# Performance work log

Measured on AMD Instinct MI355X. Metric: run time of the kernel, lower is better.

Reference implementation:

```python
import jax, jax.numpy as jnp
import numpy as np

DIM = 256
NUM_RFS = 256
OUT_DIM = 1024
N = 65536
M = 0.001


def setup_inputs() -> dict:
    key = jax.random.key(0)
    k1, k2, k3, k4, k5, k6 = jax.random.split(key, 6)
    x = jax.random.normal(k1, (N, DIM), dtype=jnp.float32)
    input_weights = jax.random.normal(k2, (OUT_DIM, DIM), dtype=jnp.float32)
    b = jax.random.normal(k3, (OUT_DIM,), dtype=jnp.float32)
    # projection matrix: normal(mean=0, std=0.02, size=(num_rfs, dim))
    proj = 0.02 * jax.random.normal(k4, (NUM_RFS, DIM), dtype=jnp.float32)
    # xis are complex points of the random-feature construction; keep small for exp stability
    xis_real = 0.1 * jax.random.normal(k5, (NUM_RFS,), dtype=jnp.float32)
    xis_imag = 0.1 * jax.random.normal(k6, (NUM_RFS,), dtype=jnp.float32)
    return {"x": x, "input_weights": input_weights, "b": b, "proj": proj,
            "xis_real": xis_real, "xis_imag": xis_imag}


def _asym_feats(xw, xis, proj, bias, is_weight):
    """create_asym_feats with a_fun/b_fun = identity, A_fun/B_fun = exp(xi*b).
    xw: (rows, DIM) float; xis: (NUM_RFS,) complex64; proj: (NUM_RFS, DIM) float.
    Returns (rows, NUM_RFS) complex64."""
    ab = xis  # ab_fun is identity -> ab_coeffs = xis
    scale = np.sqrt(1.0 + 4.0 * M).astype(np.float32)
    # renorm_gs[i] = sqrt(1+4M) * ab[i] * gs[i]  -> (NUM_RFS, DIM) complex
    renorm_gs = scale * ab[:, None] * proj.astype(jnp.complex64)
    # dot_products = xw_c @ renorm_gs.T  -> (rows, NUM_RFS) complex
    dot = jnp.einsum('nd,rd->nr', xw.astype(jnp.complex64), renorm_gs)
    sq = jnp.sum(xw * xw, axis=-1)  # (rows,)
    # correction: outer(sq/2, ab*ab) + M*||g_i||^2 (broadcast over rows)
    corr = (sq[:, None] * 0.5) * (ab * ab)[None, :]
    corr = corr + M * jnp.sum(proj * proj, axis=-1)[None, :]
    feats = jnp.exp(dot - corr) * np.float32(1.0 / np.sqrt(NUM_RFS))
    if is_weight:
        # AB_coeffs[j, i] = exp(xis[i] * bias[j])
        AB = jnp.exp(xis[None, :] * bias[:, None].astype(jnp.complex64))
        feats = AB * feats
    return feats


def reference(x, input_weights, b, proj, xis_real, xis_imag):
    xis = (xis_real + 1j * xis_imag).astype(jnp.complex64)
    # normalize=False path: scale weights and bias by dim**-0.25 at init time
    inv4 = np.float32(1.0 / DIM ** 0.25)
    w = input_weights * inv4
    bb = b * inv4
    c = np.float32((1.0 / np.sqrt(2.0)) * (1.0 + 4.0 * M) ** (DIM / 4.0))
    # precomputed weight features (parameter of the module)
    w_plus = _asym_feats(w, xis, proj, bb, is_weight=True)
    w_minus = _asym_feats(w, -xis, proj, bb, is_weight=True)
    weights = c * jnp.concatenate([w_plus, w_minus], axis=-1)  # (OUT_DIM, 2R) complex
    # forward: x scaled by 1/dim (normalize=False)
    xs = x * np.float32(1.0 / DIM)
    f_plus = _asym_feats(xs, xis, proj, bb, is_weight=False)
    f_minus = _asym_feats(xs, -xis, proj, bb, is_weight=False)
    feat = c * jnp.concatenate([f_plus, f_minus], axis=-1)  # (N, 2R) complex
    # (feat @ weights.T).real
    out = jnp.einsum('nr,or->no', feat, weights).real
    return out
```

## Files before the change

kernel.cpp:

```cpp
#include <hip/hip_runtime.h>
#include <cmath>
#include <cstdint>

#define NROWS 65536
#define DIMN  256
#define NRF   256
#define OUTD  1024
#define KDIM  1024
#define MCOEF 0.001f

typedef __bf16 v8bf __attribute__((ext_vector_type(8)));
typedef float  v4f  __attribute__((ext_vector_type(4)));
typedef unsigned short us8 __attribute__((ext_vector_type(8)));

__device__ __forceinline__ unsigned short f2bf(float f) {
  unsigned int u = __float_as_uint(f);
  u += 0x7fffu + ((u >> 16) & 1u);
  return (unsigned short)(u >> 16);
}

__device__ __forceinline__ void async_copy16(const void* g, void* l) {
  __builtin_amdgcn_global_load_lds(
      (const __attribute__((address_space(1))) void*)g,
      (__attribute__((address_space(3))) void*)l, 16, 0, 0);
}

__device__ __forceinline__ int sw_slot(int r, int c) {
  return r * 4 + ((c ^ (r >> 1)) & 3);
}

__global__ __launch_bounds__(64) void prep_rf(
    const float* __restrict__ proj, unsigned short* __restrict__ projbf,
    float* __restrict__ mg2) {
  int i = blockIdx.x;
  int lane = threadIdx.x;
  float4 v = ((const float4*)(proj + (size_t)i * DIMN))[lane];
  ushort4 o;
  o.x = f2bf(v.x); o.y = f2bf(v.y); o.z = f2bf(v.z); o.w = f2bf(v.w);
  ((ushort4*)(projbf + (size_t)i * DIMN))[lane] = o;
  float ss = v.x * v.x + v.y * v.y + v.z * v.z + v.w * v.w;
#pragma unroll
  for (int off = 32; off > 0; off >>= 1) ss += __shfl_down(ss, off, 64);
  if (lane == 0) mg2[i] = MCOEF * ss;
}

__global__ __launch_bounds__(256) void fused_features(
    const float* __restrict__ srcX,
    const float* __restrict__ srcW,
    const float* __restrict__ biasW,
    const float* __restrict__ xr_g, const float* __restrict__ xi_g,
    const float* __restrict__ mg2_g,
    const unsigned short* __restrict__ projbf,
    unsigned short* __restrict__ FX,
    unsigned short* __restrict__ FW,
    float sRx, float sRw, float scaleC) {
  __shared__ __align__(16) unsigned short big[16 * 1024];
  unsigned short* As = big;
  unsigned short* Bs = big + 2048;
  unsigned short* Os = big;
  __shared__ float xr_s[256], xi_s[256], c1_s[256], c2_s[256], mg2_s[256];
  __shared__ float sq_s[64], bias_s[64];

  int t = threadIdx.x;
  int lane = t & 63;
  int w = t >> 6;

  bool isW = blockIdx.x < (OUTD / 64);
  int blockRow = isW ? blockIdx.x * 64 : (blockIdx.x - OUTD / 64) * 64;
  const float* src = isW ? srcW : srcX;
  float scl = isW ? 0.25f : (1.f / DIMN);
  unsigned short* Fout = isW ? FW : FX;
  float sR = isW ? sRw : sRx;
  float sI = isW ? -sRw : sRx;

  {
    float a = xr_g[t], b = xi_g[t];
    xr_s[t] = a; xi_s[t] = b;
    c1_s[t] = a * a - b * b;
    c2_s[t] = 2.f * a * b;
    mg2_s[t] = mg2_g[t];
  }
  if (t < 64) bias_s[t] = isW ? biasW[blockRow + t] * 0.25f : 0.f;

  v4f acc[4][4];
#pragma unroll
  for (int a = 0; a < 4; a++)
#pragma unroll
    for (int b = 0; b < 4; b++)
#pragma unroll
      for (int q = 0; q < 4; q++) acc[a][b][q] = 0.f;

  int arow = t >> 2, sub = t & 3;
  const float* srow = src + (size_t)(blockRow + arow) * DIMN + sub * 8;
  float ss = 0.f;

  for (int kb = 0; kb < DIMN; kb += 32) {
    float4 v0 = *(const float4*)(srow + kb);
    float4 v1 = *(const float4*)(srow + kb + 4);
    v0.x *= scl; v0.y *= scl; v0.z *= scl; v0.w *= scl;
    v1.x *= scl; v1.y *= scl; v1.z *= scl; v1.w *= scl;
    ss += v0.x * v0.x + v0.y * v0.y + v0.z * v0.z + v0.w * v0.w +
          v1.x * v1.x + v1.y * v1.y + v1.z * v1.z + v1.w * v1.w;
    us8 o;
    o[0] = f2bf(v0.x); o[1] = f2bf(v0.y); o[2] = f2bf(v0.z); o[3] = f2bf(v0.w);
    o[4] = f2bf(v1.x); o[5] = f2bf(v1.y); o[6] = f2bf(v1.z); o[7] = f2bf(v1.w);
    *(us8*)&As[sw_slot(arow, sub) * 8] = o;
#pragma unroll
    for (int r = 0; r < 4; r++) {
      int idx = r * 256 + t;
      int row = idx >> 2, kc = ((idx & 3) ^ ((idx >> 3) & 3)) * 8;
      async_copy16(projbf + (size_t)row * DIMN + kb + kc,
                   Bs + (idx & ~63) * 8);
    }
    __syncthreads();
    v8bf af[4], bfv[4];
    int c = lane >> 4;
#pragma unroll
    for (int mi = 0; mi < 4; mi++)
      af[mi] = *(const v8bf*)&As[sw_slot(mi * 16 + (lane & 15), c) * 8];
#pragma unroll
    for (int ni = 0; ni < 4; ni++)
      bfv[ni] = *(const v8bf*)&Bs[sw_slot(w * 64 + ni * 16 + (lane & 15), c) * 8];
#pragma unroll
    for (int mi = 0; mi < 4; mi++)
#pragma unroll
      for (int ni = 0; ni < 4; ni++)
        acc[mi][ni] = __builtin_amdgcn_mfma_f32_16x16x32_bf16(
            af[mi], bfv[ni], acc[mi][ni], 0, 0, 0);
    __syncthreads();
  }

  ss += __shfl_xor(ss, 1, 64);
  ss += __shfl_xor(ss, 2, 64);
  if (sub == 0) sq_s[arow] = ss;

#pragma unroll
  for (int mi = 0; mi < 4; mi++) {
    __syncthreads();
#pragma unroll
    for (int ni = 0; ni < 4; ni++) {
      int i = w * 64 + ni * 16 + (lane & 15);
      float xrv = xr_s[i], xiv = xi_s[i];
      float c1v = c1_s[i], c2v = c2_s[i], mgv = mg2_s[i];
#pragma unroll
      for (int reg = 0; reg < 4; reg++) {
        int rl    = (lane >> 4) * 4 + reg;
        int rglob = mi * 16 + rl;
        float px = acc[mi][ni][reg];
        float tt = scaleC * px + bias_s[rglob];
        float u  = 0.5f * sq_s[rglob];
        float aa = u * c1v + mgv;
        float bb = u * c2v;
        float txr = tt * xrv;
        float txi = tt * xiv;
        float erp = __expf(txr - aa);
        float erm = __expf(-txr - aa);
        float s1, cc1, s2, cc2;
        __sincosf(txi - bb, &s1, &cc1);
        __sincosf(txi + bb, &s2, &cc2);
        ushort4 ov;
        ov.x = f2bf(sR * erp * cc1);
        ov.y = f2bf(sR * erm * cc2);
        ov.z = f2bf(sI * erp * s1);
        ov.w = f2bf(-sI * erm * s2);
        *(ushort4*)&Os[rl * KDIM + 4 * i] = ov;
      }
    }
    __syncthreads();
#pragma unroll
    for (int j = 0; j < 8; j++) {
      int chunk = j * 256 + t;
      int rowo  = chunk >> 7;
      int off   = (chunk & 127) * 8;
      *(us8*)(Fout + (size_t)(blockRow + mi * 16 + rowo) * KDIM + off) =
          *(const us8*)&Os[rowo * KDIM + off];
    }
  }
}

#define WAITV(N) asm volatile("s_waitcnt vmcnt(" #N ")" ::: "memory")

__global__ __launch_bounds__(512) void gemm_bt(
    const unsigned short* __restrict__ A,
    const unsigned short* __restrict__ B,
    float* __restrict__ C) {
  __shared__ __align__(16) unsigned short As[2][256 * 64];
  __shared__ __align__(16) unsigned short Bs[2][256 * 64];
  int tt = threadIdx.x;
  int lane = tt & 63;
  int wv = tt >> 6;
  int wm = wv >> 2, wn = wv & 3;

  int lid = blockIdx.x;
  int wg = (lid & 7) * 128 + (lid >> 3);
  size_t bm = (size_t)(wg >> 2) * 256;
  size_t bn = (size_t)(wg & 3) * 256;

  unsigned int offA[2][2], offB[2][2];
#pragma unroll
  for (int h = 0; h < 2; h++)
#pragma unroll
    for (int i = 0; i < 2; i++) {
      int L = i * 512 + tt;
      int rho = h * 128 + (L >> 3);
      int c = (L & 7) ^ (rho & 7);
      int gA = ((rho >> 6) & 1) * 128 + (rho >> 7) * 64 + (rho & 63);
      int gB = ((rho >> 5) & 3) * 64 + (rho >> 7) * 32 + (rho & 31);
      offA[h][i] = (unsigned int)((bm + gA) * KDIM + c * 8);
      offB[h][i] = (unsigned int)((bn + gB) * KDIM + c * 8);
    }

#define STAGE_A(H, KB) do { \
  _Pragma("unroll") for (int i_ = 0; i_ < 2; i_++) \
    async_copy16(A + offA[H][i_] + (KB), \
                 &As[nbuf][((H) * 1024 + i_ * 512 + (tt & ~63)) * 8]); \
} while (0)
#define STAGE_B(H, KB) do { \
  _Pragma("unroll") for (int i_ = 0; i_ < 2; i_++) \
    async_copy16(B + offB[H][i_] + (KB), \
                 &Bs[nbuf][((H) * 1024 + i_ * 512 + (tt & ~63)) * 8]); \
} while (0)

  v8bf af[4][2], b0[2][2], b1[2][2];
  v4f acc[8][4];
#pragma unroll
  for (int a = 0; a < 8; a++)
#pragma unroll
    for (int b = 0; b < 4; b++)
#pragma unroll
      for (int q = 0; q < 4; q++) acc[a][b][q] = 0.f;

#define READ_A(MH) do { \
  _Pragma("unroll") for (int mf_ = 0; mf_ < 4; mf_++) { \
    int rho_ = (MH) * 128 + wm * 64 + mf_ * 16 + (lane & 15); \
    int sw_ = rho_ & 7; \
    const unsigned short* rp_ = &As[buf][rho_ * 64]; \
    af[mf_][0] = *(const v8bf*)&rp_[(((lane >> 4)) ^ sw_) * 8]; \
    af[mf_][1] = *(const v8bf*)&rp_[((4 + (lane >> 4)) ^ sw_) * 8]; \
  } \
} while (0)
#define READ_B(NH, DST) do { \
  _Pragma("unroll") for (int nf_ = 0; nf_ < 2; nf_++) { \
    int rho_ = (NH) * 128 + wn * 32 + nf_ * 16 + (lane & 15); \
    int sw_ = rho_ & 7; \
    const unsigned short* rp_ = &Bs[buf][rho_ * 64]; \
    DST[nf_][0] = *(const v8bf*)&rp_[(((lane >> 4)) ^ sw_) * 8]; \
    DST[nf_][1] = *(const v8bf*)&rp_[((4 + (lane >> 4)) ^ sw_) * 8]; \
  } \
} while (0)
#define MMA_Q(MH, NH, BSRC) do { \
  __builtin_amdgcn_s_setprio(1); \
  _Pragma("unroll") for (int mf_ = 0; mf_ < 4; mf_++) \
  _Pragma("unroll") for (int nf_ = 0; nf_ < 2; nf_++) \
  _Pragma("unroll") for (int ks_ = 0; ks_ < 2; ks_++) \
    acc[(MH) * 4 + mf_][(NH) * 2 + nf_] = \
        __builtin_amdgcn_mfma_f32_16x16x32_bf16( \
            af[mf_][ks_], BSRC[nf_][ks_], \
            acc[(MH) * 4 + mf_][(NH) * 2 + nf_], 0, 0, 0); \
  __builtin_amdgcn_s_setprio(0); \
} while (0)

  {
    const int nbuf = 0;
    STAGE_A(0, 0); STAGE_B(0, 0); STAGE_B(1, 0); STAGE_A(1, 0);
  }
  WAITV(4);
  __builtin_amdgcn_s_barrier();

  for (int t = 0; t < 16; ++t) {
    const int buf = t & 1, nbuf = buf ^ 1;
    const bool pf = (t < 15);
    const int kb = (t + 1) * 64;

    READ_A(0); READ_B(0, b0);
    if (pf) STAGE_A(0, kb);
    __builtin_amdgcn_s_barrier();
    MMA_Q(0, 0, b0);
    if (pf) { WAITV(4); } else { WAITV(2); }
    __builtin_amdgcn_s_barrier();

    READ_B(1, b1);
    if (pf) STAGE_B(0, kb);
    __builtin_amdgcn_s_barrier();
    MMA_Q(0, 1, b1);
    if (pf) { WAITV(4); } else { WAITV(0); }
    __builtin_amdgcn_s_barrier();

    READ_A(1);
    if (pf) STAGE_B(1, kb);
    __builtin_amdgcn_s_barrier();
    MMA_Q(1, 1, b1);
    __builtin_amdgcn_s_barrier();

    if (pf) STAGE_A(1, kb);
    __builtin_amdgcn_s_barrier();
    MMA_Q(1, 0, b0);
    if (pf) { WAITV(4); }
    __builtin_amdgcn_s_barrier();
  }

#pragma unroll
  for (int mf = 0; mf < 8; mf++)
#pragma unroll
    for (int nf = 0; nf < 4; nf++)
#pragma unroll
      for (int reg = 0; reg < 4; reg++) {
        size_t row = bm + wm * 128 + mf * 16 + (lane >> 4) * 4 + reg;
        size_t col = bn + wn * 64 + nf * 16 + (lane & 15);
        C[row * OUTD + col] = acc[mf][nf][reg];
      }
#undef STAGE_A
#undef STAGE_B
#undef READ_A
#undef READ_B
#undef MMA_Q
}

extern "C" void kernel_launch(void* const* d_in, const int* in_sizes, int n_in,
                              void* d_out, int out_size, void* d_ws, size_t ws_size,
                              hipStream_t stream) {
  (void)in_sizes; (void)n_in; (void)out_size;
  const float* x    = (const float*)d_in[0];
  const float* iw   = (const float*)d_in[1];
  const float* bvec = (const float*)d_in[2];
  const float* proj = (const float*)d_in[3];
  const float* xr   = (const float*)d_in[4];
  const float* xi   = (const float*)d_in[5];
  float* out = (float*)d_out;

  char* ws = (char*)d_ws;
  size_t off = 0;
  auto take = [&](size_t bytes) {
    char* p = ws + off;
    off = (off + bytes + 255) & ~(size_t)255;
    return p;
  };
  unsigned short* F      = (unsigned short*)take((size_t)NROWS * KDIM * 2);
  unsigned short* Wp     = (unsigned short*)take((size_t)OUTD * KDIM * 2);
  unsigned short* projbf = (unsigned short*)take((size_t)NRF * DIMN * 2);
  float* mg2 = (float*)take((size_t)NRF * 4);
  if (ws_size < off) return;

  const float  scaleC = sqrtf(1.f + 4.f * MCOEF);
  const double c2d    = 0.5 * exp(128.0 * log(1.0 + 4.0 * 0.001));
  const float  invSR  = 0.0625f;
  const float  sRw    = (float)(c2d * 0.0625);

  prep_rf<<<NRF, 64, 0, stream>>>(proj, projbf, mg2);
  fused_features<<<NROWS / 64 + OUTD / 64, 256, 0, stream>>>(
      x, iw, bvec, xr, xi, mg2, projbf, F, Wp, invSR, sRw, scaleC);
  gemm_bt<<<1024, 512, 0, stream>>>(F, Wp, out);
}
```

Before: 506.8 us.

## Double-buffer feature-kernel K loop and store features directly to global

Splits the A and B LDS tiles of the fused feature kernel into two buffers. The next K slice can then be staged while MFMAs run on the current one, removing one barrier per iteration. It also drops the LDS staging of the bf16 output tile and writes each 8-byte feature group straight to global memory, removing the per-row-block barriers and LDS round trip. The trade-offs are more LDS per block, which may lower occupancy, and narrower, less coalesced global stores.

```diff
diff --git a/kernel.cpp b/kernel.cpp
--- a/kernel.cpp
+++ b/kernel.cpp
@@ -54,10 +54,8 @@
     unsigned short* __restrict__ FX,
     unsigned short* __restrict__ FW,
     float sRx, float sRw, float scaleC) {
-  __shared__ __align__(16) unsigned short big[16 * 1024];
-  unsigned short* As = big;
-  unsigned short* Bs = big + 2048;
-  unsigned short* Os = big;
+  __shared__ __align__(16) unsigned short As[2][64 * 32];
+  __shared__ __align__(16) unsigned short Bs[2][256 * 32];
   __shared__ float xr_s[256], xi_s[256], c1_s[256], c2_s[256], mg2_s[256];
   __shared__ float sq_s[64], bias_s[64];
 
@@ -94,7 +92,16 @@
   const float* srow = src + (size_t)(blockRow + arow) * DIMN + sub * 8;
   float ss = 0.f;
 
-  for (int kb = 0; kb < DIMN; kb += 32) {
+  auto stageB = [&](int nb, int kb) {
+#pragma unroll
+    for (int r = 0; r < 4; r++) {
+      int idx = r * 256 + t;
+      int row = idx >> 2, kc = ((idx & 3) ^ ((idx >> 3) & 3)) * 8;
+      async_copy16(projbf + (size_t)row * DIMN + kb + kc,
+                   &Bs[nb][(idx & ~63) * 8]);
+    }
+  };
+  auto stageA = [&](int nb, int kb) {
     float4 v0 = *(const float4*)(srow + kb);
     float4 v1 = *(const float4*)(srow + kb + 4);
     v0.x *= scl; v0.y *= scl; v0.z *= scl; v0.w *= scl;
@@ -104,23 +111,27 @@
     us8 o;
     o[0] = f2bf(v0.x); o[1] = f2bf(v0.y); o[2] = f2bf(v0.z); o[3] = f2bf(v0.w);
     o[4] = f2bf(v1.x); o[5] = f2bf(v1.y); o[6] = f2bf(v1.z); o[7] = f2bf(v1.w);
-    *(us8*)&As[sw_slot(arow, sub) * 8] = o;
-#pragma unroll
-    for (int r = 0; r < 4; r++) {
-      int idx = r * 256 + t;
-      int row = idx >> 2, kc = ((idx & 3) ^ ((idx >> 3) & 3)) * 8;
-      async_copy16(projbf + (size_t)row * DIMN + kb + kc,
-                   Bs + (idx & ~63) * 8);
+    *(us8*)&As[nb][sw_slot(arow, sub) * 8] = o;
+  };
+
+  stageB(0, 0);
+  stageA(0, 0);
+  __syncthreads();
+
+  for (int kb = 0; kb < 8; kb++) {
+    int cur = kb & 1, nb = cur ^ 1;
+    if (kb < 7) {
+      stageB(nb, (kb + 1) * 32);
+      stageA(nb, (kb + 1) * 32);
     }
-    __syncthreads();
     v8bf af[4], bfv[4];
     int c = lane >> 4;
 #pragma unroll
     for (int mi = 0; mi < 4; mi++)
-      af[mi] = *(const v8bf*)&As[sw_slot(mi * 16 + (lane & 15), c) * 8];
+      af[mi] = *(const v8bf*)&As[cur][sw_slot(mi * 16 + (lane & 15), c) * 8];
 #pragma unroll
     for (int ni = 0; ni < 4; ni++)
-      bfv[ni] = *(const v8bf*)&Bs[sw_slot(w * 64 + ni * 16 + (lane & 15), c) * 8];
+      bfv[ni] = *(const v8bf*)&Bs[cur][sw_slot(w * 64 + ni * 16 + (lane & 15), c) * 8];
 #pragma unroll
     for (int mi = 0; mi < 4; mi++)
 #pragma unroll
@@ -133,10 +144,10 @@
   ss += __shfl_xor(ss, 1, 64);
   ss += __shfl_xor(ss, 2, 64);
   if (sub == 0) sq_s[arow] = ss;
-
-#pragma unroll
-  for (int mi = 0; mi < 4; mi++) {
-    __syncthreads();
+  __syncthreads();
+
+#pragma unroll
+  for (int mi = 0; mi < 4; mi++)
 #pragma unroll
     for (int ni = 0; ni < 4; ni++) {
       int i = w * 64 + ni * 16 + (lane & 15);
@@ -144,8 +155,7 @@
       float c1v = c1_s[i], c2v = c2_s[i], mgv = mg2_s[i];
 #pragma unroll
       for (int reg = 0; reg < 4; reg++) {
-        int rl    = (lane >> 4) * 4 + reg;
-        int rglob = mi * 16 + rl;
+        int rglob = mi * 16 + (lane >> 4) * 4 + reg;
         float px = acc[mi][ni][reg];
         float tt = scaleC * px + bias_s[rglob];
         float u  = 0.5f * sq_s[rglob];
@@ -163,19 +173,9 @@
         ov.y = f2bf(sR * erm * cc2);
         ov.z = f2bf(sI * erp * s1);
         ov.w = f2bf(-sI * erm * s2);
-        *(ushort4*)&Os[rl * KDIM + 4 * i] = ov;
+        *(ushort4*)(Fout + (size_t)(blockRow + rglob) * KDIM + 4 * i) = ov;
       }
     }
-    __syncthreads();
-#pragma unroll
-    for (int j = 0; j < 8; j++) {
-      int chunk = j * 256 + t;
-      int rowo  = chunk >> 7;
-      int off   = (chunk & 127) * 8;
-      *(us8*)(Fout + (size_t)(blockRow + mi * 16 + rowo) * KDIM + off) =
-          *(const us8*)&Os[rowo * KDIM + off];
-    }
-  }
 }
 
 #define WAITV(N) asm volatile("s_waitcnt vmcnt(" #N ")" ::: "memory")
```

Measured after the change: 497.0 us. No clear change (-2.0%).
